# Optimization experiments

Hardware: AMD Instinct MI355X
Metric: run time of the kernel (lower is better)

Reference implementation:

```python
import jax, jax.numpy as jnp
import numpy as np

B, N, C = 8, 1024, 768
DIM_HEAD = 32
NUM_HEADS = C // DIM_HEAD  # 24


def setup_inputs() -> dict:
    key = jax.random.key(0)
    ks = jax.random.split(key, 6)
    s = 0.02
    return {
        "x": jax.random.normal(ks[0], (B, N, C), dtype=jnp.float32),
        "shared_rel_pos": jax.random.normal(ks[1], (NUM_HEADS, N, N), dtype=jnp.float32),
        "Wqkv": jax.random.normal(ks[2], (3 * C, C), dtype=jnp.float32) * s,
        "bqkv": jax.random.normal(ks[3], (3 * C,), dtype=jnp.float32) * s,
        "Wproj": jax.random.normal(ks[4], (C, C), dtype=jnp.float32) * s,
        "bproj": jax.random.normal(ks[5], (C,), dtype=jnp.float32) * s,
    }


def reference(x, shared_rel_pos, Wqkv, bqkv, Wproj, bproj):
    b, n, c = x.shape
    h, dh = NUM_HEADS, DIM_HEAD
    scale = dh ** -0.5
    # qkv projection: [B,N,3C] -> view as [B,N,H,3*dh] (head_first layout)
    qkv = (jnp.einsum('bnc,oc->bno', x, Wqkv) + bqkv).reshape(b, n, h, 3 * dh)
    qkv = jnp.transpose(qkv, (0, 2, 1, 3))          # [B,H,N,3*dh]
    q, k, v = jnp.split(qkv, 3, axis=-1)            # each [B,H,N,dh]
    attn = jnp.einsum('bhqd,bhkd->bhqk', q * scale, k)  # [B,H,N,N]
    attn = attn + shared_rel_pos[None]              # broadcast bias [H,N,N]
    attn = jax.nn.softmax(attn, axis=-1)
    out = jnp.einsum('bhqk,bhkd->bhqd', attn, v)    # [B,H,N,dh]
    out = jnp.transpose(out, (0, 2, 1, 3)).reshape(b, n, h * dh)
    return jnp.einsum('bnc,oc->bno', out, Wproj) + bproj
```

## Files before the change

### kernel.cpp

```cpp
#include <hip/hip_runtime.h>

typedef __bf16 bf16_t;
typedef __bf16 bf16x8 __attribute__((ext_vector_type(8)));
typedef __bf16 bf16x4 __attribute__((ext_vector_type(4)));
typedef float f32x4 __attribute__((ext_vector_type(4)));
typedef unsigned int u32;
typedef u32 u32x2 __attribute__((ext_vector_type(2)));
typedef u32 u32x4 __attribute__((ext_vector_type(4)));

#define MFMA16(a, b, c) __builtin_amdgcn_mfma_f32_16x16x32_bf16(a, b, c, 0, 0, 0)

#if __has_builtin(__builtin_amdgcn_exp2f)
#define EXP2(x) __builtin_amdgcn_exp2f(x)
#else
#define EXP2(x) exp2f(x)
#endif

#if __has_builtin(__builtin_amdgcn_permlane32_swap) && __has_builtin(__builtin_amdgcn_permlane16_swap)
#define PERMSWAP(a, b)                                                     \
  do {                                                                     \
    u32x2 _r = __builtin_amdgcn_permlane32_swap((a), (b), false, false);   \
    u32x2 _s = __builtin_amdgcn_permlane16_swap(_r[0], _r[1], false, false); \
    (a) = _s[0];                                                           \
    (b) = _s[1];                                                           \
  } while (0)
#else
#define PERMSWAP(a, b)                                                     \
  do {                                                                     \
    asm("v_permlane32_swap_b32 %0, %1" : "+v"(b), "+v"(a));                \
    asm("v_permlane16_swap_b32 %0, %1" : "+v"(b), "+v"(a));                \
  } while (0)
#endif

__device__ __forceinline__ void g2l16(const void* g, void* l) {
  __builtin_amdgcn_global_load_lds(
      (__attribute__((address_space(1))) void*)g,
      (__attribute__((address_space(3))) void*)l, 16, 0, 0);
}

__global__ void cvt_f32_bf16(const float* __restrict__ in, bf16_t* __restrict__ out, int n4) {
  int i = blockIdx.x * blockDim.x + threadIdx.x;
  if (i >= n4) return;
  const float4 v = ((const float4*)in)[i];
  bf16x4 o;
  o[0] = (bf16_t)v.x; o[1] = (bf16_t)v.y; o[2] = (bf16_t)v.z; o[3] = (bf16_t)v.w;
  ((bf16x4*)out)[i] = o;
}

__global__ void permute_rel(const float* __restrict__ rel, bf16_t* __restrict__ relp) {
  __shared__ bf16_t Tl[16][1032];
  const int blk = blockIdx.x;
  const int h = blk >> 6, qt = blk & 63;
  const int t = threadIdx.x;
  const float LOG2E = 1.44269504f;
  const float* src = rel + ((size_t)h * 1024 + qt * 16) * 1024;
#pragma unroll
  for (int it = 0; it < 16; ++it) {
    const int fid = it * 256 + t;
    const int row = fid >> 8, c4 = (fid & 255) * 4;
    const float4 v = *(const float4*)(src + (size_t)row * 1024 + c4);
    bf16x4 o;
    o[0] = (bf16_t)(v.x * LOG2E); o[1] = (bf16_t)(v.y * LOG2E);
    o[2] = (bf16_t)(v.z * LOG2E); o[3] = (bf16_t)(v.w * LOG2E);
    *(bf16x4*)&Tl[row][c4] = o;
  }
  __syncthreads();
  bf16_t* dst = relp + (size_t)blk * 16384;
#pragma unroll
  for (int s = 0; s < 8; ++s) {
    const int c = s * 256 + t;
    const int kb = c >> 8, i = (c >> 6) & 3, lane = c & 63;
    const int lr = lane & 15, quad = lane >> 4;
    bf16x8 o;
#pragma unroll
    for (int j = 0; j < 8; ++j) {
      const int k = kb * 128 + (2 * i + (j >> 2)) * 16 + quad * 4 + (j & 3);
      o[j] = Tl[lr][k];
    }
    *(bf16x8*)(dst + (size_t)c * 8) = o;
  }
}

__global__ void transpose_v(const bf16_t* __restrict__ Vb, bf16_t* __restrict__ Vtb) {
  __shared__ bf16_t T[64][40];
  const int bh = blockIdx.y, s0 = blockIdx.x * 64;
  const int r = threadIdx.x >> 2, c8 = (threadIdx.x & 3) * 8;
  const bf16x8 v = *(const bf16x8*)(Vb + ((size_t)bh * 1024 + s0 + r) * 32 + c8);
#pragma unroll
  for (int j = 0; j < 8; ++j) T[r][c8 + j] = v[j];
  __syncthreads();
  const int d = threadIdx.x >> 3, q8 = (threadIdx.x & 7) * 8;
  bf16x8 o;
#pragma unroll
  for (int j = 0; j < 8; ++j) o[j] = T[q8 + j][d];
  *(bf16x8*)(Vtb + ((size_t)bh * 32 + d) * 1024 + s0 + q8) = o;
}

template <int MODE>
__global__ __launch_bounds__(256, 3) void gemm_bt(
    const bf16_t* __restrict__ A, const bf16_t* __restrict__ Bw,
    const float* __restrict__ bias, float* __restrict__ Cout,
    bf16_t* __restrict__ Qb, bf16_t* __restrict__ Kb, bf16_t* __restrict__ Vb,
    int M, int N, int K) {
  __shared__ bf16_t As[2][128 * 32];
  __shared__ bf16_t Bs[2][128 * 32];
  const int tid = threadIdx.x;
  const int wave = tid >> 6, lane = tid & 63, quad = lane >> 4, lr = lane & 15;
  const int bm = blockIdx.x * 128, bn = blockIdx.y * 128;
  const int wm = (wave >> 1) * 64, wn = (wave & 1) * 64;

  f32x4 acc[4][4] = {};

  const bf16_t* Ag;
  size_t strideA64;
  if (MODE == 0) {
    Ag = A + (size_t)(bm + (tid >> 2)) * K + (tid & 3) * 8;
    strideA64 = (size_t)64 * K;
  } else {
    const int rr = bm + (tid >> 2);
    const int bidx = rr >> 10, seq = rr & 1023;
    Ag = A + ((size_t)bidx * 24 * 1024 + seq) * 32 + (tid & 3) * 8;
    strideA64 = (size_t)64 * 32;
  }
  const bf16_t* Bg = Bw + (size_t)(bn + (tid >> 2)) * K + (tid & 3) * 8;
  const size_t strideB64 = (size_t)64 * K;

  auto stage = [&](int k0, int sel) {
    const size_t aoff = (MODE == 0) ? (size_t)k0 : (size_t)(k0 >> 5) * 32768;
    g2l16(Ag + aoff, &As[sel][tid * 8]);
    g2l16(Ag + strideA64 + aoff, &As[sel][tid * 8 + 2048]);
    g2l16(Bg + k0, &Bs[sel][tid * 8]);
    g2l16(Bg + strideB64 + k0, &Bs[sel][tid * 8 + 2048]);
  };

  const int NT = K >> 5;
  stage(0, 0);
  __syncthreads();
  for (int t = 0; t < NT; ++t) {
    const int sel = t & 1;
    if (t + 1 < NT) stage((t + 1) * 32, sel ^ 1);
    bf16x8 af[4], bfr[4];
#pragma unroll
    for (int i = 0; i < 4; ++i)
      af[i] = *(const bf16x8*)(&As[sel][(wm + i * 16 + lr) * 32 + quad * 8]);
#pragma unroll
    for (int j = 0; j < 4; ++j)
      bfr[j] = *(const bf16x8*)(&Bs[sel][(wn + j * 16 + lr) * 32 + quad * 8]);
#pragma unroll
    for (int i = 0; i < 4; ++i)
#pragma unroll
      for (int j = 0; j < 4; ++j)
        acc[i][j] = MFMA16(af[i], bfr[j], acc[i][j]);
    __syncthreads();
  }

#pragma unroll
  for (int i = 0; i < 4; ++i) {
    const int row = bm + wm + i * 16 + quad * 4;
#pragma unroll
    for (int j = 0; j < 4; ++j) {
      const int col = bn + wn + j * 16 + lr;
      const float bb = bias[col];
#pragma unroll
      for (int r = 0; r < 4; ++r) {
        const float v = acc[i][j][r] + bb;
        const int rr = row + r;
        if (MODE == 1) {
          Cout[(size_t)rr * N + col] = v;
        } else {
          const int b = rr >> 10, seq = rr & 1023;
          const int head = col / 96, w = col % 96;
          const int bh = b * 24 + head;
          if (w < 32) {
            Qb[((size_t)bh * 1024 + seq) * 32 + w] = (bf16_t)(v * 0.17677669529663687f);
          } else if (w < 64) {
            Kb[((size_t)bh * 1024 + seq) * 32 + (w - 32)] = (bf16_t)v;
          } else {
            Vb[((size_t)bh * 1024 + seq) * 32 + (w - 64)] = (bf16_t)v;
          }
        }
      }
    }
  }
}

__global__ __launch_bounds__(256, 4) void attn_flash(
    const bf16_t* __restrict__ Qb, const bf16_t* __restrict__ Kb,
    const bf16_t* __restrict__ Vtb, const bf16_t* __restrict__ relp,
    bf16_t* __restrict__ Ob) {
  __shared__ bf16_t Ks[2][128 * 32];
  __shared__ bf16_t Vs[2][32 * 128];

  const int tid = threadIdx.x;
  const int wave = tid >> 6, lane = tid & 63, quad = lane >> 4, lr = lane & 15;

  const int flat = blockIdx.x;
  const int xcd = flat & 7, slot = flat >> 3;
  const int pair = xcd + 8 * (slot >> 4);
  const int qi = slot & 15;
  const int b = pair / 24, h = pair % 24;
  const int bh = b * 24 + h;
  const int q0 = qi * 64 + wave * 16;
  const float LOG2E = 1.44269504f;

  const bf16x8 qf = *(const bf16x8*)(Qb + ((size_t)bh * 1024 + q0 + lr) * 32 + quad * 8);

  bf16x8 onesf;
#pragma unroll
  for (int i = 0; i < 8; ++i) onesf[i] = (bf16_t)1.0f;

  f32x4 o_acc[2] = {};
  f32x4 l_acc = {};

  const bf16_t* relg = relp + (size_t)(h * 64 + qi * 4 + wave) * 16384 + lane * 8;
  const bf16_t* Kg = Kb + (size_t)bh * 1024 * 32;
  const bf16_t* Vg = Vtb + (size_t)bh * 32 * 1024;

  auto stageKV = [&](int kt, int sel) {
#pragma unroll
    for (int p = 0; p < 2; ++p) {
      const int cid = p * 256 + tid;
      const int krow = cid >> 2, kc = cid & 3;
      const int ks_ = (krow >> 1) & 3;
      g2l16(Kg + ((size_t)(kt + krow) * 32 + ((kc ^ ks_) * 8)), &Ks[sel][cid * 8]);
      const int vd = cid >> 4, vc = cid & 15;
      g2l16(Vg + ((size_t)vd * 1024 + kt + ((vc ^ (vd & 7)) * 8)), &Vs[sel][cid * 8]);
    }
  };

  auto body = [&](int kt, int sel) {
    bf16x8 bb[4];
    const bf16_t* rb = relg + (size_t)(kt >> 7) * 2048;
#pragma unroll
    for (int i = 0; i < 4; ++i) bb[i] = *(const bf16x8*)(rb + i * 512);

    f32x4 s[8];
    const f32x4 zz = {0.f, 0.f, 0.f, 0.f};
    const int kcs = quad ^ ((lr >> 1) & 3);
#pragma unroll
    for (int jt = 0; jt < 8; ++jt) {
      const bf16x8 kf = *(const bf16x8*)&Ks[sel][(jt * 16 + lr) * 32 + kcs * 8];
      s[jt] = MFMA16(kf, qf, zz);
    }
#pragma unroll
    for (int jt = 0; jt < 8; ++jt)
#pragma unroll
      for (int r = 0; r < 4; ++r)
        s[jt][r] = EXP2(fmaf(s[jt][r], LOG2E, (float)bb[jt >> 1][(jt & 1) * 4 + r]));

#pragma unroll
    for (int ks = 0; ks < 4; ++ks) {
      bf16x4 pe, po;
#pragma unroll
      for (int r = 0; r < 4; ++r) {
        pe[r] = (bf16_t)s[2 * ks][r];
        po[r] = (bf16_t)s[2 * ks + 1][r];
      }
      u32x2 ue = __builtin_bit_cast(u32x2, pe);
      u32x2 uo = __builtin_bit_cast(u32x2, po);
      u32 d0 = ue[0], d1 = ue[1], d2 = uo[0], d3 = uo[1];
      PERMSWAP(d0, d2);
      PERMSWAP(d1, d3);
      u32x4 uf = {d0, d1, d2, d3};
      const bf16x8 pf = __builtin_bit_cast(bf16x8, uf);

      l_acc = MFMA16(pf, onesf, l_acc);
#pragma unroll
      for (int nt = 0; nt < 2; ++nt) {
        const int d = nt * 16 + lr;
        const int vc = (ks * 4 + quad) ^ (d & 7);
        const bf16x8 vf = *(const bf16x8*)&Vs[sel][d * 128 + vc * 8];
        o_acc[nt] = MFMA16(pf, vf, o_acc[nt]);
      }
    }
  };

  stageKV(0, 0);
  __syncthreads();
  for (int t = 0; t < 8; ++t) {
    const int sel = t & 1;
    if (t < 7) stageKV((t + 1) * 128, sel ^ 1);
    body(t * 128, sel);
    __syncthreads();
  }

  float inv_l[4];
#pragma unroll
  for (int r = 0; r < 4; ++r) inv_l[r] = 1.0f / l_acc[r];
#pragma unroll
  for (int nt = 0; nt < 2; ++nt)
#pragma unroll
    for (int r = 0; r < 4; ++r) {
      const int seq = q0 + quad * 4 + r;
      Ob[((size_t)bh * 1024 + seq) * 32 + nt * 16 + lr] = (bf16_t)(o_acc[nt][r] * inv_l[r]);
    }
}

extern "C" void kernel_launch(void* const* d_in, const int* in_sizes, int n_in,
                              void* d_out, int out_size, void* d_ws, size_t ws_size,
                              hipStream_t stream) {
  const float* x = (const float*)d_in[0];
  const float* rel = (const float*)d_in[1];
  const float* Wqkv = (const float*)d_in[2];
  const float* bqkv = (const float*)d_in[3];
  const float* Wproj = (const float*)d_in[4];
  const float* bproj = (const float*)d_in[5];
  float* out = (float*)d_out;

  char* ws = (char*)d_ws;
  bf16_t* xb = (bf16_t*)ws;     ws += (size_t)8192 * 768 * 2;
  bf16_t* wqkvb = (bf16_t*)ws;  ws += (size_t)2304 * 768 * 2;
  bf16_t* wprojb = (bf16_t*)ws; ws += (size_t)768 * 768 * 2;
  bf16_t* Qb = (bf16_t*)ws;     ws += (size_t)192 * 1024 * 32 * 2;
  bf16_t* Kb = (bf16_t*)ws;     ws += (size_t)192 * 1024 * 32 * 2;
  bf16_t* Vb = (bf16_t*)ws;     ws += (size_t)192 * 1024 * 32 * 2;
  bf16_t* Vtb = (bf16_t*)ws;    ws += (size_t)192 * 1024 * 32 * 2;
  bf16_t* relp = (bf16_t*)ws;   ws += (size_t)24 * 1024 * 1024 * 2;
  bf16_t* Ob = xb;

  cvt_f32_bf16<<<(8192 * 768 / 4 + 255) / 256, 256, 0, stream>>>(x, xb, 8192 * 768 / 4);
  cvt_f32_bf16<<<(2304 * 768 / 4 + 255) / 256, 256, 0, stream>>>(Wqkv, wqkvb, 2304 * 768 / 4);
  cvt_f32_bf16<<<(768 * 768 / 4 + 255) / 256, 256, 0, stream>>>(Wproj, wprojb, 768 * 768 / 4);
  permute_rel<<<dim3(24 * 64), 256, 0, stream>>>(rel, relp);

  gemm_bt<0><<<dim3(64, 18), 256, 0, stream>>>(xb, wqkvb, bqkv, nullptr,
                                               Qb, Kb, Vb, 8192, 2304, 768);
  transpose_v<<<dim3(16, 192), 256, 0, stream>>>(Vb, Vtb);
  attn_flash<<<dim3(3072), 256, 0, stream>>>(Qb, Kb, Vtb, relp, Ob);
  gemm_bt<1><<<dim3(64, 6), 256, 0, stream>>>(Ob, wprojb, bproj, out,
                                              nullptr, nullptr, nullptr, 8192, 768, 768);
}
```

Measured before the change: 329.3 us.

## Fuse V transpose into QKV GEMM epilogue and vectorize output stores

Swaps the MFMA operand order so each lane holds four consecutive output columns, which allows float4 and bf16x4 stores in the GEMM epilogue in place of scalar writes. V is now written directly in transposed [bh][d][seq] layout from the QKV GEMM, removing the transpose_v kernel launch and its intermediate buffer round-trip. The transposed V stores are scalar and strided by 1024 elements, so those writes are less coalesced than the Q and K stores.

```diff
diff --git a/kernel.cpp b/kernel.cpp
--- a/kernel.cpp
+++ b/kernel.cpp
@@ -81,26 +81,11 @@
   }
 }
 
-__global__ void transpose_v(const bf16_t* __restrict__ Vb, bf16_t* __restrict__ Vtb) {
-  __shared__ bf16_t T[64][40];
-  const int bh = blockIdx.y, s0 = blockIdx.x * 64;
-  const int r = threadIdx.x >> 2, c8 = (threadIdx.x & 3) * 8;
-  const bf16x8 v = *(const bf16x8*)(Vb + ((size_t)bh * 1024 + s0 + r) * 32 + c8);
-#pragma unroll
-  for (int j = 0; j < 8; ++j) T[r][c8 + j] = v[j];
-  __syncthreads();
-  const int d = threadIdx.x >> 3, q8 = (threadIdx.x & 7) * 8;
-  bf16x8 o;
-#pragma unroll
-  for (int j = 0; j < 8; ++j) o[j] = T[q8 + j][d];
-  *(bf16x8*)(Vtb + ((size_t)bh * 32 + d) * 1024 + s0 + q8) = o;
-}
-
 template <int MODE>
 __global__ __launch_bounds__(256, 3) void gemm_bt(
     const bf16_t* __restrict__ A, const bf16_t* __restrict__ Bw,
     const float* __restrict__ bias, float* __restrict__ Cout,
-    bf16_t* __restrict__ Qb, bf16_t* __restrict__ Kb, bf16_t* __restrict__ Vb,
+    bf16_t* __restrict__ Qb, bf16_t* __restrict__ Kb, bf16_t* __restrict__ Vtb,
     int M, int N, int K) {
   __shared__ bf16_t As[2][128 * 32];
   __shared__ bf16_t Bs[2][128 * 32];
@@ -150,34 +135,43 @@
     for (int i = 0; i < 4; ++i)
 #pragma unroll
       for (int j = 0; j < 4; ++j)
-        acc[i][j] = MFMA16(af[i], bfr[j], acc[i][j]);
+        acc[i][j] = MFMA16(bfr[j], af[i], acc[i][j]);
     __syncthreads();
   }
 
 #pragma unroll
-  for (int i = 0; i < 4; ++i) {
-    const int row = bm + wm + i * 16 + quad * 4;
-#pragma unroll
-    for (int j = 0; j < 4; ++j) {
-      const int col = bn + wn + j * 16 + lr;
-      const float bb = bias[col];
-#pragma unroll
-      for (int r = 0; r < 4; ++r) {
-        const float v = acc[i][j][r] + bb;
-        const int rr = row + r;
-        if (MODE == 1) {
-          Cout[(size_t)rr * N + col] = v;
+  for (int j = 0; j < 4; ++j) {
+    const int col0 = bn + wn + j * 16 + quad * 4;
+    const float4 bb = *(const float4*)(bias + col0);
+#pragma unroll
+    for (int i = 0; i < 4; ++i) {
+      const int row = bm + wm + i * 16 + lr;
+      const float v0 = acc[i][j][0] + bb.x, v1 = acc[i][j][1] + bb.y;
+      const float v2 = acc[i][j][2] + bb.z, v3 = acc[i][j][3] + bb.w;
+      if (MODE == 1) {
+        float4 o = {v0, v1, v2, v3};
+        *(float4*)(Cout + (size_t)row * N + col0) = o;
+      } else {
+        const int b = row >> 10, seq = row & 1023;
+        const int head = col0 / 96, w0 = col0 % 96;
+        const int bh = b * 24 + head;
+        if (w0 < 32) {
+          const float sc = 0.17677669529663687f;
+          bf16x4 q4;
+          q4[0] = (bf16_t)(v0 * sc); q4[1] = (bf16_t)(v1 * sc);
+          q4[2] = (bf16_t)(v2 * sc); q4[3] = (bf16_t)(v3 * sc);
+          *(bf16x4*)(Qb + ((size_t)bh * 1024 + seq) * 32 + w0) = q4;
+        } else if (w0 < 64) {
+          bf16x4 k4;
+          k4[0] = (bf16_t)v0; k4[1] = (bf16_t)v1;
+          k4[2] = (bf16_t)v2; k4[3] = (bf16_t)v3;
+          *(bf16x4*)(Kb + ((size_t)bh * 1024 + seq) * 32 + (w0 - 32)) = k4;
         } else {
-          const int b = rr >> 10, seq = rr & 1023;
-          const int head = col / 96, w = col % 96;
-          const int bh = b * 24 + head;
-          if (w < 32) {
-            Qb[((size_t)bh * 1024 + seq) * 32 + w] = (bf16_t)(v * 0.17677669529663687f);
-          } else if (w < 64) {
-            Kb[((size_t)bh * 1024 + seq) * 32 + (w - 32)] = (bf16_t)v;
-          } else {
-            Vb[((size_t)bh * 1024 + seq) * 32 + (w - 64)] = (bf16_t)v;
-          }
+          bf16_t* vp = Vtb + ((size_t)bh * 32 + (w0 - 64)) * 1024 + seq;
+          vp[0] = (bf16_t)v0;
+          vp[1024] = (bf16_t)v1;
+          vp[2048] = (bf16_t)v2;
+          vp[3072] = (bf16_t)v3;
         }
       }
     }
@@ -313,7 +307,6 @@
   bf16_t* wprojb = (bf16_t*)ws; ws += (size_t)768 * 768 * 2;
   bf16_t* Qb = (bf16_t*)ws;     ws += (size_t)192 * 1024 * 32 * 2;
   bf16_t* Kb = (bf16_t*)ws;     ws += (size_t)192 * 1024 * 32 * 2;
-  bf16_t* Vb = (bf16_t*)ws;     ws += (size_t)192 * 1024 * 32 * 2;
   bf16_t* Vtb = (bf16_t*)ws;    ws += (size_t)192 * 1024 * 32 * 2;
   bf16_t* relp = (bf16_t*)ws;   ws += (size_t)24 * 1024 * 1024 * 2;
   bf16_t* Ob = xb;
@@ -324,8 +317,7 @@
   permute_rel<<<dim3(24 * 64), 256, 0, stream>>>(rel, relp);
 
   gemm_bt<0><<<dim3(64, 18), 256, 0, stream>>>(xb, wqkvb, bqkv, nullptr,
-                                               Qb, Kb, Vb, 8192, 2304, 768);
-  transpose_v<<<dim3(16, 192), 256, 0, stream>>>(Vb, Vtb);
+                                               Qb, Kb, Vtb, 8192, 2304, 768);
   attn_flash<<<dim3(3072), 256, 0, stream>>>(Qb, Kb, Vtb, relp, Ob);
   gemm_bt<1><<<dim3(64, 6), 256, 0, stream>>>(Ob, wprojb, bproj, out,
                                               nullptr, nullptr, nullptr, 8192, 768, 768);
```

Result: no change. 325.7 us (-1.1%).
